# Optimization experiments

Hardware: AMD Instinct MI355X
Metric: run time of the kernel (lower is better)

The kernel has to match this reference:

```python
import jax, jax.numpy as jnp
import numpy as np

EPS = 1e-5
TEMP = 0.2  # contrastive temperature


def setup_inputs() -> dict:
    key = jax.random.key(0)
    ks_ = jax.random.split(key, 16)
    N, d, d_free, D, F_ = 10000, 32, 32, 64, 3
    x = jax.random.normal(ks_[0], (N, 256), dtype=jnp.float32)
    feats = jax.random.normal(ks_[1], (F_, N, d), dtype=jnp.float32)
    feat_free = 0.01 * jax.random.normal(ks_[2], (N, d_free), dtype=jnp.float32)
    # curvatures: k = init_curvature * randn(); keep away from 0 so the curved branch is taken
    ks = jax.random.uniform(ks_[3], (F_,), dtype=jnp.float32) + 0.5
    Ws = jax.random.normal(ks_[4], (F_, D, d), dtype=jnp.float32)
    Ws = Ws / jnp.linalg.norm(Ws, axis=-1, keepdims=True)  # row-normalized as in __init__
    bias = 2.0 * jnp.pi * jax.random.uniform(ks_[5], (F_, D), dtype=jnp.float32)
    W_free = jax.random.normal(ks_[6], (D, d_free), dtype=jnp.float32)
    W_free = W_free / jnp.linalg.norm(W_free, axis=-1, keepdims=True)
    b_free = 2.0 * jnp.pi * jax.random.uniform(ks_[7], (D,), dtype=jnp.float32)
    W1 = 0.05 * jax.random.normal(ks_[8], (3 * d, 64), dtype=jnp.float32)
    b1 = jnp.zeros((64,), dtype=jnp.float32)
    W2 = 0.05 * jax.random.normal(ks_[9], (64, 1), dtype=jnp.float32)
    b2 = jnp.zeros((1,), dtype=jnp.float32)
    motif = jax.random.randint(ks_[10], (3, 50000), 0, N, dtype=jnp.int32)
    neg_uv = jax.random.randint(ks_[11], (2, 50000), 0, N, dtype=jnp.int32)
    return {"x": x, "feats": feats, "feat_free": feat_free, "ks": ks,
            "Ws": Ws, "bias": bias, "W_free": W_free, "b_free": b_free,
            "W1": W1, "b1": b1, "W2": W2, "b2": b2,
            "motif": motif, "neg_uv": neg_uv}


def _normalize(xf, k):
    # RiemannianFeatures.normalize with the random scale fixed at 0.5 for determinism
    radius = 1.0 / jnp.sqrt(jnp.abs(k))
    xn = jnp.linalg.norm(xf, axis=-1, keepdims=True)
    return xf / xn * (0.9 * 0.5) * radius


def _mlp(f3, W1, b1, W2, b2):
    return jax.nn.relu(f3 @ W1 + b1) @ W2 + b2  # [M, 1]


def _gather3(feat, m):
    # nodes_from_motif: concat features of u, v, w
    return jnp.concatenate([feat[m[0]], feat[m[1]], feat[m[2]]], axis=-1)


def reference(x, feats, feat_free, ks, Ws, bias, W_free, b_free,
              W1, b1, W2, b2, motif, neg_uv):
    F_, N, d = feats.shape
    d_free = feat_free.shape[-1]

    # ---- RiemannianFeatures.forward: normalized products per factor + free part
    products = [_normalize(feats[i], ks[i]) for i in range(F_)]
    products.append(feat_free)

    # ---- random_mapping: pairwise manifold distance -> exp/cos transform
    zs = []
    for i in range(F_):
        xi, w, b, k = products[i], Ws[i], bias[i], ks[i]
        div = jnp.sum((xi[:, None, :] - w[None, :, :]) ** 2, axis=-1)      # [N, D]
        num = 1.0 + k * jnp.sum(xi * xi, axis=-1, keepdims=True)           # [N, 1]
        dist = jnp.log(num / (div + EPS))
        zs.append(jnp.exp((d - 1) * dist * 0.5) * jnp.cos(dist + b))
    dist_f = feat_free @ W_free.T                                          # Euclidean branch
    zs.append(jnp.exp((d_free - 1) * dist_f * 0.5) * jnp.cos(dist_f + b_free))
    x2 = jnp.concatenate(zs, axis=-1)                                      # [N, embed]

    # ---- cal_cl_loss: full N x N cosine-similarity contrastive loss
    n1 = jnp.linalg.norm(x, axis=-1)
    n2 = jnp.linalg.norm(x2, axis=-1)
    sim = jnp.einsum('ik,jk->ij', x, x2) / (n1[:, None] * n2[None, :])
    sim = jnp.exp(sim / TEMP)
    pos = jnp.diagonal(sim)
    loss_1 = -jnp.mean(jnp.log(pos / (jnp.sum(sim, axis=0) - pos)))
    loss_2 = -jnp.mean(jnp.log(pos / (jnp.sum(sim, axis=1) - pos)))
    cl_loss = 0.5 * (loss_1 + loss_2)

    # ---- cal_motif_loss: gather triples -> MLP -> BCE (neg via provided sampled pairs)
    neg_motif = jnp.concatenate([neg_uv, motif[2:3]], axis=0)
    motif_loss = jnp.float32(0.0)
    for p in products:
        pos_logit = _mlp(_gather3(p, motif), W1, b1, W2, b2)
        neg_logit = _mlp(_gather3(p, neg_motif), W1, b1, W2, b2)
        motif_loss = motif_loss \
            - jnp.mean(jax.nn.log_sigmoid(pos_logit)) \
            - jnp.mean(jax.nn.log_sigmoid(-neg_logit))

    return cl_loss + motif_loss
```

## Files before the change

### kernel.cpp

```cpp
#include <hip/hip_runtime.h>
#include <hip/hip_bf16.h>
#include <math.h>

#define EMBED 256
#define NF 3
#define DD 64
#define BM 128
#define BN 128
#define BK 64
#define NKT 4
#define MOTIF_BLOCKS 2048

typedef unsigned short ushort_t;
typedef unsigned char uchar_t;
typedef float f32x4 __attribute__((ext_vector_type(4)));
typedef float f32x2 __attribute__((ext_vector_type(2)));

__device__ __forceinline__ void gl2lds16(const void* g, void* l) {
    __builtin_amdgcn_global_load_lds(
        (const __attribute__((address_space(1))) unsigned int*)g,
        (__attribute__((address_space(3))) unsigned int*)l, 16, 0, 0);
}

__device__ __forceinline__ uchar_t f2fp8(float f) {
    int p = __builtin_amdgcn_cvt_pk_fp8_f32(f, f, 0, false);
    return (uchar_t)(p & 0xff);
}
template<bool HI>
__device__ __forceinline__ f32x2 pk2(unsigned int w) {
    return __builtin_amdgcn_cvt_pk_f32_fp8((int)w, HI);
}

__device__ __forceinline__ float dpp16_red_add(float x) {
    int v;
    v = __builtin_amdgcn_update_dpp(0, __float_as_int(x), 0xB1, 0xF, 0xF, true);
    x += __int_as_float(v);
    v = __builtin_amdgcn_update_dpp(0, __float_as_int(x), 0x4E, 0xF, 0xF, true);
    x += __int_as_float(v);
    v = __builtin_amdgcn_update_dpp(0, __float_as_int(x), 0x141, 0xF, 0xF, true);
    x += __int_as_float(v);
    v = __builtin_amdgcn_update_dpp(0, __float_as_int(x), 0x140, 0xF, 0xF, true);
    x += __int_as_float(v);
    return x;
}

__global__ __launch_bounds__(256) void k_embed(
    const float* __restrict__ x,
    const float* __restrict__ feats,
    const float* __restrict__ feat_free,
    const float* __restrict__ ks,
    const float* __restrict__ Ws,
    const float* __restrict__ bias,
    const float* __restrict__ W_free,
    const float* __restrict__ b_free,
    float* __restrict__ p_out,
    uchar_t* __restrict__ xnf8,
    uchar_t* __restrict__ x2nf8,
    float* __restrict__ acc3,
    int N, int Npad)
{
    int tid  = threadIdx.x;
    int wave = tid >> 6;
    int t    = tid & 63;
    int gtid = blockIdx.x * 256 + tid;
    int stride = gridDim.x * 256;

    for (int i = gtid; i < 4; i += stride) acc3[i] = 0.f;
    {
        int pad = (Npad - N) * (EMBED/4);
        int* pa = (int*)(xnf8  + (size_t)N*EMBED);
        int* pb = (int*)(x2nf8 + (size_t)N*EMBED);
        for (int i = gtid; i < pad; i += stride) { pa[i] = 0; pb[i] = 0; }
    }

    __shared__ float Wl[128*65];
    __shared__ float xi_s[4][NF][32];
    __shared__ float ff_s[4][32];

    for (int e = tid; e < NF*DD*32; e += 256) {
        int i = e >> 11, rem = e & 2047, tr = rem >> 5, c = rem & 31;
        Wl[(i*32 + c)*65 + tr] = Ws[e];
    }
    for (int e = tid; e < DD*32; e += 256) {
        int tr = e >> 5, c = e & 31;
        Wl[(96 + c)*65 + tr] = W_free[e];
    }
    __syncthreads();

    float (*xi)[32] = xi_s[wave];
    float* ffs = ff_s[wave];
    int ngroups = (N + 3) >> 2;

    for (int grp = blockIdx.x; grp < ngroups; grp += gridDim.x) {
        int n = grp*4 + wave;
        if (n >= N) continue;

        float v[NF];
        float ffv = 0.f;
        if (t < 32) {
            #pragma unroll
            for (int i = 0; i < NF; ++i) v[i] = feats[((size_t)i*N + n)*32 + t];
            ffv = feat_free[(size_t)n*32 + t];
        } else {
            #pragma unroll
            for (int i = 0; i < NF; ++i) v[i] = 0.f;
        }

        float num[NF];
        #pragma unroll
        for (int i = 0; i < NF; ++i) {
            float s = v[i]*v[i];
            s += __shfl_xor(s, 1, 64);  s += __shfl_xor(s, 2, 64);
            s += __shfl_xor(s, 4, 64);  s += __shfl_xor(s, 8, 64);
            s += __shfl_xor(s, 16, 64);
            s = __shfl(s, 0, 64);
            float k = ks[i];
            float scale = 0.45f / (sqrtf(s) * sqrtf(fabsf(k)));
            float xv = v[i] * scale;
            if (t < 32) {
                xi[i][t] = xv;
                p_out[((size_t)i*N + n)*32 + t] = xv;
            }
            num[i] = 1.0f + k * (scale*scale*s);
        }
        if (t < 32) ffs[t] = ffv;

        float z[4];
        float zsq = 0.f;
        #pragma unroll
        for (int i = 0; i < NF; ++i) {
            float div = 0.f;
            #pragma unroll
            for (int c = 0; c < 32; ++c) {
                float d = xi[i][c] - Wl[(i*32 + c)*65 + t];
                div += d*d;
            }
            float dist = __logf(num[i] / (div + 1e-5f));
            float zz = __expf(15.5f * dist) * __cosf(dist + bias[i*DD + t]);
            z[i] = zz;
            zsq += zz*zz;
        }
        {
            float dot = 0.f;
            #pragma unroll
            for (int c = 0; c < 32; ++c) dot = fmaf(ffs[c], Wl[(96 + c)*65 + t], dot);
            float zz = __expf(15.5f * dot) * __cosf(dot + b_free[t]);
            z[3] = zz;
            zsq += zz*zz;
        }
        zsq += __shfl_xor(zsq, 1, 64);  zsq += __shfl_xor(zsq, 2, 64);
        zsq += __shfl_xor(zsq, 4, 64);  zsq += __shfl_xor(zsq, 8, 64);
        zsq += __shfl_xor(zsq, 16, 64); zsq += __shfl_xor(zsq, 32, 64);
        float iv2 = 1.0f / sqrtf(zsq);

        #pragma unroll
        for (int i = 0; i < NF; ++i) x2nf8[(size_t)n*EMBED + i*DD + t] = f2fp8(z[i]*iv2);
        x2nf8[(size_t)n*EMBED + 192 + t] = f2fp8(z[3]*iv2);

        float xv[4];
        float s1 = 0.f;
        #pragma unroll
        for (int q = 0; q < 4; ++q) { xv[q] = x[(size_t)n*EMBED + q*64 + t]; s1 += xv[q]*xv[q]; }
        s1 += __shfl_xor(s1, 1, 64);  s1 += __shfl_xor(s1, 2, 64);
        s1 += __shfl_xor(s1, 4, 64);  s1 += __shfl_xor(s1, 8, 64);
        s1 += __shfl_xor(s1, 16, 64); s1 += __shfl_xor(s1, 32, 64);
        float iv1 = 5.0f / sqrtf(s1);
        #pragma unroll
        for (int q = 0; q < 4; ++q) xnf8[(size_t)n*EMBED + q*64 + t] = f2fp8(xv[q]*iv1);
    }
}

__global__ __launch_bounds__(256) void k_mlp1(
    const float* __restrict__ p,
    const float* __restrict__ feat_free,
    const float* __restrict__ W1,
    const float* __restrict__ b1,
    uchar_t* __restrict__ H,
    int N)
{
    int lane = threadIdx.x & 63;
    int gw = (blockIdx.x * blockDim.x + threadIdx.x) >> 6;
    int nwaves = (gridDim.x * blockDim.x) >> 6;

    float wcol[96];
    #pragma unroll
    for (int c = 0; c < 96; ++c) wcol[c] = W1[c*64 + lane];
    float b1l = b1[lane];

    int total = 4 * N;
    for (int unit = gw; unit < total; unit += nwaves) {
        int node = __builtin_amdgcn_readfirstlane(unit >> 2);
        int prod = __builtin_amdgcn_readfirstlane(unit & 3);
        const float* P = (prod < 3) ? (p + ((size_t)prod*N + node)*32)
                                    : (feat_free + (size_t)node*32);
        float fc[32];
        #pragma unroll
        for (int c = 0; c < 32; ++c) fc[c] = P[c];
        #pragma unroll
        for (int s = 0; s < 3; ++s) {
            float h = (s == 2) ? b1l : 0.f;
            #pragma unroll
            for (int c = 0; c < 32; ++c) h = fmaf(fc[c], wcol[s*32 + c], h);
            H[(((size_t)prod*3 + s)*N + node)*64 + lane] = f2fp8(h);
        }
    }
}

__global__ __launch_bounds__(256, 4) void k_fused(
    const uchar_t* __restrict__ xn, const uchar_t* __restrict__ x2n,
    const uchar_t* __restrict__ H,
    const int* __restrict__ motif,
    const int* __restrict__ neg_uv,
    const float* __restrict__ W2,
    const float* __restrict__ b2,
    float* __restrict__ rowpart,
    float* __restrict__ colpart,
    float* __restrict__ pos,
    float* __restrict__ partials,
    int N, int Npad, int nb, int M)
{
    __shared__ __align__(16) uchar_t smem[2*(BM*BK + BN*BK)];

    if (blockIdx.x < MOTIF_BLOCKS) {
        float* wred = (float*)smem;
        int lane = threadIdx.x & 63;
        int sub  = lane >> 3;
        int ch   = (lane & 7) * 8;
        int caseId = blockIdx.x & 7;
        int rank   = (blockIdx.x >> 3) * 4 + (threadIdx.x >> 6);
        int prod  = caseId >> 1;
        int isneg = caseId & 1;
        const uchar_t* Hu = H + ((size_t)prod*3 + 0)*N*64;
        const uchar_t* Hv = H + ((size_t)prod*3 + 1)*N*64;
        const uchar_t* Hw = H + ((size_t)prod*3 + 2)*N*64;
        const int* iu = isneg ? neg_uv       : motif;
        const int* iv = isneg ? (neg_uv + M) : (motif + M);
        const int* iw = motif + 2*M;

        float w2c[8];
        #pragma unroll
        for (int c = 0; c < 8; ++c) w2c[c] = W2[ch + c];
        float b2v = b2[0];

        float accl = 0.f;
        #pragma unroll 2
        for (int r0 = rank*8; r0 < M; r0 += 8192) {
            int r = r0 + sub;
            bool ok = (r < M);
            int rc = ok ? r : 0;
            int u = iu[rc], v = iv[rc], w = iw[rc];
            uint2 du = *(const uint2*)&Hu[(size_t)u*64 + ch];
            uint2 dv = *(const uint2*)&Hv[(size_t)v*64 + ch];
            uint2 dw = *(const uint2*)&Hw[(size_t)w*64 + ch];
            float pl = 0.f;
            {
                f32x2 s;
                s = pk2<false>(du.x) + pk2<false>(dv.x) + pk2<false>(dw.x);
                pl = fmaf(fmaxf(s.x,0.f), w2c[0], pl);  pl = fmaf(fmaxf(s.y,0.f), w2c[1], pl);
                s = pk2<true>(du.x) + pk2<true>(dv.x) + pk2<true>(dw.x);
                pl = fmaf(fmaxf(s.x,0.f), w2c[2], pl);  pl = fmaf(fmaxf(s.y,0.f), w2c[3], pl);
                s = pk2<false>(du.y) + pk2<false>(dv.y) + pk2<false>(dw.y);
                pl = fmaf(fmaxf(s.x,0.f), w2c[4], pl);  pl = fmaf(fmaxf(s.y,0.f), w2c[5], pl);
                s = pk2<true>(du.y) + pk2<true>(dv.y) + pk2<true>(dw.y);
                pl = fmaf(fmaxf(s.x,0.f), w2c[6], pl);  pl = fmaf(fmaxf(s.y,0.f), w2c[7], pl);
            }
            pl += __shfl_xor(pl, 1, 64);
            pl += __shfl_xor(pl, 2, 64);
            pl += __shfl_xor(pl, 4, 64);
            float logit = pl + b2v;
            float z = isneg ? -logit : logit;
            float sp = fmaxf(-z, 0.f) + __logf(1.f + __expf(-fabsf(z)));
            accl -= ok ? sp : 0.f;
        }
        #pragma unroll
        for (int m = 1; m < 64; m <<= 1) accl += __shfl_xor(accl, m, 64);

        if (lane == 0) wred[threadIdx.x >> 6] = accl;
        __syncthreads();
        if (threadIdx.x == 0)
            partials[blockIdx.x] = (wred[0] + wred[1] + wred[2] + wred[3]) * 0.125f;
        return;
    }

    int tid  = threadIdx.x;
    int lane = tid & 63;
    int w    = tid >> 6;
    int wr   = w >> 1, wc = w & 1;
    int quad = lane >> 4, l15 = lane & 15;

    int pid = blockIdx.x - MOTIF_BLOCKS;
    int nwg = nb * nb;
    int qq = nwg >> 3, rr = nwg & 7;
    int xcd = pid & 7, idx = pid >> 3;
    int wg = (xcd < rr ? xcd*(qq+1) : rr*(qq+1) + (xcd-rr)*qq) + idx;

    int per_group = 8 * nb;
    int group = wg / per_group;
    int rem = wg - group * per_group;
    int rowspan = min(8, nb - group * 8);
    int prow = group * 8 + rem % rowspan;
    int pcol = rem / rowspan;
    int row0 = prow * BM, col0 = pcol * BN;

    f32x4 acc[4][4];
    #pragma unroll
    for (int i = 0; i < 4; ++i)
        #pragma unroll
        for (int j = 0; j < 4; ++j) acc[i][j] = (f32x4){0.f,0.f,0.f,0.f};

    auto stage = [&](int t) {
        uchar_t* A = smem + (t & 1) * (BM*BK + BN*BK);
        uchar_t* B = A + BM*BK;
        int k0 = t * BK;
        #pragma unroll
        for (int i = 0; i < 2; ++i) {
            int slot = i*256 + tid;
            int r = slot >> 2, c = slot & 3;
            int sc = c ^ ((r >> 1) & 3);
            gl2lds16(xn  + (size_t)(row0 + r)*EMBED + k0 + sc*16, &A[slot*16]);
            gl2lds16(x2n + (size_t)(col0 + r)*EMBED + k0 + sc*16, &B[slot*16]);
        }
    };

    stage(0);
    stage(1);

    #pragma unroll
    for (int kt = 0; kt < NKT; ++kt) {
        if (kt == NKT-1) asm volatile("s_waitcnt vmcnt(0)" ::: "memory");
        else             asm volatile("s_waitcnt vmcnt(4)" ::: "memory");
        __builtin_amdgcn_s_barrier();

        const uchar_t* A = smem + (kt & 1) * (BM*BK + BN*BK);
        const uchar_t* B = A + BM*BK;
        #pragma unroll
        for (int s = 0; s < 2; ++s) {
            long a[4], b[4];
            int cq = s*2 + (quad >> 1);
            int h8 = (quad & 1) * 8;
            #pragma unroll
            for (int ti = 0; ti < 4; ++ti) {
                int ra = wr*64 + ti*16 + l15;
                a[ti] = *(const long*)&A[ra*BK + ((cq ^ ((ra >> 1) & 3)) << 4) + h8];
            }
            #pragma unroll
            for (int tj = 0; tj < 4; ++tj) {
                int rb = wc*64 + tj*16 + l15;
                b[tj] = *(const long*)&B[rb*BK + ((cq ^ ((rb >> 1) & 3)) << 4) + h8];
            }
            __builtin_amdgcn_s_setprio(1);
            #pragma unroll
            for (int ti = 0; ti < 4; ++ti)
                #pragma unroll
                for (int tj = 0; tj < 4; ++tj)
                    acc[ti][tj] = __builtin_amdgcn_mfma_f32_16x16x32_fp8_fp8(a[ti], b[tj], acc[ti][tj], 0, 0, 0);
            __builtin_amdgcn_s_setprio(0);
        }
        if (kt + 2 < NKT) {
            __builtin_amdgcn_s_barrier();
            stage(kt + 2);
        }
    }
    __syncthreads();

    float* rsum_s = (float*)smem;
    float* csum_s = rsum_s + 2*BM;

    bool edge = (prow == nb-1) || (pcol == nb-1);
    float csv[4] = {0.f, 0.f, 0.f, 0.f};

    if (!edge) {
        bool diagb = (prow == pcol) && (wr == wc);
        #pragma unroll
        for (int ti = 0; ti < 4; ++ti) {
            #pragma unroll
            for (int r = 0; r < 4; ++r) {
                float rs = 0.f;
                #pragma unroll
                for (int tj = 0; tj < 4; ++tj) {
                    float e = __expf(acc[ti][tj][r]);
                    rs += e;
                    csv[tj] += e;
                    if (tj == ti && diagb && l15 == quad*4 + r)
                        pos[row0 + wr*64 + ti*16 + quad*4 + r] = e;
                }
                rs = dpp16_red_add(rs);
                if (l15 == 0) rsum_s[wc*BM + wr*64 + ti*16 + quad*4 + r] = rs;
            }
        }
    } else {
        #pragma unroll
        for (int ti = 0; ti < 4; ++ti) {
            #pragma unroll
            for (int r = 0; r < 4; ++r) {
                int gi = row0 + wr*64 + ti*16 + quad*4 + r;
                float rs = 0.f;
                #pragma unroll
                for (int tj = 0; tj < 4; ++tj) {
                    int gj = col0 + wc*64 + tj*16 + l15;
                    float e = 0.f;
                    if (gi < N && gj < N) {
                        e = __expf(acc[ti][tj][r]);
                        if (gi == gj) pos[gi] = e;
                    }
                    rs += e;
                    csv[tj] += e;
                }
                rs = dpp16_red_add(rs);
                if (l15 == 0) rsum_s[wc*BM + wr*64 + ti*16 + quad*4 + r] = rs;
            }
        }
    }
    #pragma unroll
    for (int tj = 0; tj < 4; ++tj) {
        float cs = csv[tj];
        cs += __shfl_xor(cs, 16, 64);
        cs += __shfl_xor(cs, 32, 64);
        if (lane < 16) csum_s[wr*BM + wc*64 + tj*16 + lane] = cs;
    }
    __syncthreads();
    if (tid < BM) {
        rowpart[(size_t)pcol*Npad + row0 + tid] = rsum_s[tid] + rsum_s[BM + tid];
        colpart[(size_t)prow*Npad + col0 + tid] = csum_s[tid] + csum_s[BM + tid];
    }
}

__global__ __launch_bounds__(256) void k_final(
    const float* __restrict__ rowpart, const float* __restrict__ colpart,
    const float* __restrict__ pos, const float* __restrict__ partials,
    float* __restrict__ acc3, int* __restrict__ ticket,
    float* __restrict__ out, int N, int Npad, int nb, int nparts, int M)
{
    __shared__ float red1[256], red2[256], red3[256];
    int t = threadIdx.x;
    int g = blockIdx.x * 256 + t;
    int stride = gridDim.x * 256;
    float l1 = 0.f, l2 = 0.f, mo = 0.f;
    for (int i = g; i < N; i += stride) {
        float rs = 0.f, cs = 0.f;
        for (int p = 0; p < nb; ++p) {
            rs += rowpart[(size_t)p*Npad + i];
            cs += colpart[(size_t)p*Npad + i];
        }
        float pv = pos[i];
        l1 += __logf((cs - pv) / pv);
        l2 += __logf((rs - pv) / pv);
    }
    for (int i = g; i < nparts; i += stride) mo += partials[i];
    red1[t] = l1; red2[t] = l2; red3[t] = mo; __syncthreads();
    for (int s = 128; s > 0; s >>= 1) {
        if (t < s) { red1[t] += red1[t+s]; red2[t] += red2[t+s]; red3[t] += red3[t+s]; }
        __syncthreads();
    }
    if (t == 0) {
        atomicAdd(&acc3[0], red1[0]);
        atomicAdd(&acc3[1], red2[0]);
        atomicAdd(&acc3[2], red3[0]);
        __threadfence();
        int old = atomicAdd(ticket, 1);
        if (old == (int)gridDim.x - 1) {
            float a0 = atomicAdd(&acc3[0], 0.f);
            float a1 = atomicAdd(&acc3[1], 0.f);
            float a2 = atomicAdd(&acc3[2], 0.f);
            float cl = 0.5f * (a0 + a1) / (float)N;
            out[0] = cl - a2 / (float)M;
        }
    }
}

extern "C" void kernel_launch(void* const* d_in, const int* in_sizes, int n_in,
                              void* d_out, int out_size, void* d_ws, size_t ws_size,
                              hipStream_t stream)
{
    const float* x         = (const float*)d_in[0];
    const float* feats     = (const float*)d_in[1];
    const float* feat_free = (const float*)d_in[2];
    const float* ks        = (const float*)d_in[3];
    const float* Ws        = (const float*)d_in[4];
    const float* bias      = (const float*)d_in[5];
    const float* W_free    = (const float*)d_in[6];
    const float* b_free    = (const float*)d_in[7];
    const float* W1        = (const float*)d_in[8];
    const float* b1        = (const float*)d_in[9];
    const float* W2        = (const float*)d_in[10];
    const float* b2        = (const float*)d_in[11];
    const int*   motif     = (const int*)d_in[12];
    const int*   neg_uv    = (const int*)d_in[13];
    int N = in_sizes[0] / EMBED;
    int M = in_sizes[13] / 2;
    int nb = (N + BM - 1) / BM;
    int Npad = nb * BM;

    uchar_t* xnf8  = (uchar_t*)d_ws;
    uchar_t* x2nf8 = xnf8 + (size_t)Npad*EMBED;
    uchar_t* H8    = x2nf8 + (size_t)Npad*EMBED;
    float* p      = (float*)(H8 + (size_t)12*N*64);
    float* posv   = p + (size_t)3*N*32;
    float* acc3   = posv + N;
    int*   ticket = (int*)(acc3 + 3);
    float* partials = acc3 + 4;
    float* rowpart  = partials + MOTIF_BLOCKS;
    float* colpart  = rowpart + (size_t)nb*Npad;

    k_embed<<<512, 256, 0, stream>>>(x, feats, feat_free, ks, Ws, bias,
                                     W_free, b_free, p, xnf8, x2nf8,
                                     acc3, N, Npad);
    k_mlp1<<<1024, 256, 0, stream>>>(p, feat_free, W1, b1, H8, N);
    k_fused<<<MOTIF_BLOCKS + nb*nb, 256, 0, stream>>>(xnf8, x2nf8, H8, motif, neg_uv,
                                                      W2, b2, rowpart, colpart, posv,
                                                      partials, N, Npad, nb, M);
    k_final<<<64, 256, 0, stream>>>(rowpart, colpart, posv, partials, acc3, ticket,
                                    (float*)d_out, N, Npad, nb, MOTIF_BLOCKS, M);
}
```

Before: 219.6 us.

## Expand squared distance algebraically, hold weights in registers, use readlane broadcasts

The embed kernel no longer stages the weight matrices in LDS. Each lane keeps its own weight row in registers, broadcasts the node features with readlane, and computes the squared distance as |x|^2 - 2x·w + |w|^2 from a precomputed row norm instead of summing squared differences. This removes the LDS staging, block barrier and per-element subtracts, but raises register pressure and may lose some precision through cancellation. Wave reductions now use DPP, and the final reduction kernel launches 256 blocks instead of 64.

```diff
diff --git a/kernel.cpp b/kernel.cpp
--- a/kernel.cpp
+++ b/kernel.cpp
@@ -29,6 +29,10 @@
 template<bool HI>
 __device__ __forceinline__ f32x2 pk2(unsigned int w) {
     return __builtin_amdgcn_cvt_pk_f32_fp8((int)w, HI);
+}
+
+__device__ __forceinline__ float lanef(float v, int l) {
+    return __int_as_float(__builtin_amdgcn_readlane(__float_as_int(v), l));
 }
 
 __device__ __forceinline__ float dpp16_red_add(float x) {
@@ -41,6 +45,12 @@
     x += __int_as_float(v);
     v = __builtin_amdgcn_update_dpp(0, __float_as_int(x), 0x140, 0xF, 0xF, true);
     x += __int_as_float(v);
+    return x;
+}
+__device__ __forceinline__ float red64_add(float x) {
+    x = dpp16_red_add(x);
+    x += __shfl_xor(x, 16, 64);
+    x += __shfl_xor(x, 32, 64);
     return x;
 }
 
@@ -73,24 +83,40 @@
         for (int i = gtid; i < pad; i += stride) { pa[i] = 0; pb[i] = 0; }
     }
 
-    __shared__ float Wl[128*65];
-    __shared__ float xi_s[4][NF][32];
-    __shared__ float ff_s[4][32];
-
-    for (int e = tid; e < NF*DD*32; e += 256) {
-        int i = e >> 11, rem = e & 2047, tr = rem >> 5, c = rem & 31;
-        Wl[(i*32 + c)*65 + tr] = Ws[e];
-    }
-    for (int e = tid; e < DD*32; e += 256) {
-        int tr = e >> 5, c = e & 31;
-        Wl[(96 + c)*65 + tr] = W_free[e];
-    }
-    __syncthreads();
-
-    float (*xi)[32] = xi_s[wave];
-    float* ffs = ff_s[wave];
+    float Wr[NF][32], Wf[32];
+    #pragma unroll
+    for (int i = 0; i < NF; ++i) {
+        const f32x4* src = (const f32x4*)(Ws + ((size_t)i*DD + t)*32);
+        #pragma unroll
+        for (int q = 0; q < 8; ++q) {
+            f32x4 v4 = src[q];
+            Wr[i][q*4+0] = v4[0]; Wr[i][q*4+1] = v4[1];
+            Wr[i][q*4+2] = v4[2]; Wr[i][q*4+3] = v4[3];
+        }
+    }
+    {
+        const f32x4* src = (const f32x4*)(W_free + (size_t)t*32);
+        #pragma unroll
+        for (int q = 0; q < 8; ++q) {
+            f32x4 v4 = src[q];
+            Wf[q*4+0] = v4[0]; Wf[q*4+1] = v4[1];
+            Wf[q*4+2] = v4[2]; Wf[q*4+3] = v4[3];
+        }
+    }
+    float wn2[NF];
+    #pragma unroll
+    for (int i = 0; i < NF; ++i) {
+        float s = 0.f;
+        #pragma unroll
+        for (int c = 0; c < 32; ++c) s = fmaf(Wr[i][c], Wr[i][c], s);
+        wn2[i] = s;
+    }
+    float kv[NF], bi[NF];
+    #pragma unroll
+    for (int i = 0; i < NF; ++i) { kv[i] = ks[i]; bi[i] = bias[i*DD + t]; }
+    float bf = b_free[t];
+
     int ngroups = (N + 3) >> 2;
-
     for (int grp = blockIdx.x; grp < ngroups; grp += gridDim.x) {
         int n = grp*4 + wave;
         if (n >= N) continue;
@@ -106,67 +132,57 @@
             for (int i = 0; i < NF; ++i) v[i] = 0.f;
         }
 
-        float num[NF];
+        float xv[NF], sq[NF], num[NF];
         #pragma unroll
         for (int i = 0; i < NF; ++i) {
-            float s = v[i]*v[i];
-            s += __shfl_xor(s, 1, 64);  s += __shfl_xor(s, 2, 64);
-            s += __shfl_xor(s, 4, 64);  s += __shfl_xor(s, 8, 64);
-            s += __shfl_xor(s, 16, 64);
-            s = __shfl(s, 0, 64);
-            float k = ks[i];
-            float scale = 0.45f / (sqrtf(s) * sqrtf(fabsf(k)));
-            float xv = v[i] * scale;
-            if (t < 32) {
-                xi[i][t] = xv;
-                p_out[((size_t)i*N + n)*32 + t] = xv;
-            }
-            num[i] = 1.0f + k * (scale*scale*s);
-        }
-        if (t < 32) ffs[t] = ffv;
+            float s = red64_add(v[i]*v[i]);
+            float scale = 0.45f / (sqrtf(s) * sqrtf(fabsf(kv[i])));
+            xv[i] = v[i] * scale;
+            sq[i] = scale*scale*s;
+            num[i] = 1.0f + kv[i] * sq[i];
+            if (t < 32) p_out[((size_t)i*N + n)*32 + t] = xv[i];
+        }
+
+        float dot[NF] = {0.f, 0.f, 0.f};
+        float dotf = 0.f;
+        #pragma unroll
+        for (int c = 0; c < 32; ++c) {
+            dot[0] = fmaf(lanef(xv[0], c), Wr[0][c], dot[0]);
+            dot[1] = fmaf(lanef(xv[1], c), Wr[1][c], dot[1]);
+            dot[2] = fmaf(lanef(xv[2], c), Wr[2][c], dot[2]);
+            dotf   = fmaf(lanef(ffv,   c), Wf[c],    dotf);
+        }
 
         float z[4];
         float zsq = 0.f;
         #pragma unroll
         for (int i = 0; i < NF; ++i) {
-            float div = 0.f;
-            #pragma unroll
-            for (int c = 0; c < 32; ++c) {
-                float d = xi[i][c] - Wl[(i*32 + c)*65 + t];
-                div += d*d;
-            }
+            float div = sq[i] - 2.f*dot[i] + wn2[i];
             float dist = __logf(num[i] / (div + 1e-5f));
-            float zz = __expf(15.5f * dist) * __cosf(dist + bias[i*DD + t]);
+            float zz = __expf(15.5f * dist) * __cosf(dist + bi[i]);
             z[i] = zz;
             zsq += zz*zz;
         }
         {
-            float dot = 0.f;
-            #pragma unroll
-            for (int c = 0; c < 32; ++c) dot = fmaf(ffs[c], Wl[(96 + c)*65 + t], dot);
-            float zz = __expf(15.5f * dot) * __cosf(dot + b_free[t]);
+            float zz = __expf(15.5f * dotf) * __cosf(dotf + bf);
             z[3] = zz;
             zsq += zz*zz;
         }
-        zsq += __shfl_xor(zsq, 1, 64);  zsq += __shfl_xor(zsq, 2, 64);
-        zsq += __shfl_xor(zsq, 4, 64);  zsq += __shfl_xor(zsq, 8, 64);
-        zsq += __shfl_xor(zsq, 16, 64); zsq += __shfl_xor(zsq, 32, 64);
+        zsq = red64_add(zsq);
         float iv2 = 1.0f / sqrtf(zsq);
 
         #pragma unroll
         for (int i = 0; i < NF; ++i) x2nf8[(size_t)n*EMBED + i*DD + t] = f2fp8(z[i]*iv2);
         x2nf8[(size_t)n*EMBED + 192 + t] = f2fp8(z[3]*iv2);
 
-        float xv[4];
+        float xvv[4];
         float s1 = 0.f;
         #pragma unroll
-        for (int q = 0; q < 4; ++q) { xv[q] = x[(size_t)n*EMBED + q*64 + t]; s1 += xv[q]*xv[q]; }
-        s1 += __shfl_xor(s1, 1, 64);  s1 += __shfl_xor(s1, 2, 64);
-        s1 += __shfl_xor(s1, 4, 64);  s1 += __shfl_xor(s1, 8, 64);
-        s1 += __shfl_xor(s1, 16, 64); s1 += __shfl_xor(s1, 32, 64);
+        for (int q = 0; q < 4; ++q) { xvv[q] = x[(size_t)n*EMBED + q*64 + t]; s1 += xvv[q]*xvv[q]; }
+        s1 = red64_add(s1);
         float iv1 = 5.0f / sqrtf(s1);
         #pragma unroll
-        for (int q = 0; q < 4; ++q) xnf8[(size_t)n*EMBED + q*64 + t] = f2fp8(xv[q]*iv1);
+        for (int q = 0; q < 4; ++q) xnf8[(size_t)n*EMBED + q*64 + t] = f2fp8(xvv[q]*iv1);
     }
 }
 
@@ -509,6 +525,6 @@
     k_fused<<<MOTIF_BLOCKS + nb*nb, 256, 0, stream>>>(xnf8, x2nf8, H8, motif, neg_uv,
                                                       W2, b2, rowpart, colpart, posv,
                                                       partials, N, Npad, nb, M);
-    k_final<<<64, 256, 0, stream>>>(rowpart, colpart, posv, partials, acc3, ticket,
-                                    (float*)d_out, N, Npad, nb, MOTIF_BLOCKS, M);
-}
+    k_final<<<256, 256, 0, stream>>>(rowpart, colpart, posv, partials, acc3, ticket,
+                                     (float*)d_out, N, Npad, nb, MOTIF_BLOCKS, M);
+}
```

New measurement: 227.6 us. 3.6% more time.
